# Kernel optimization log

Measured on AMD Instinct MI355X. Metric: run time of the kernel, lower is better.

The kernel has to match this reference:

```python
import jax, jax.numpy as jnp
import numpy as np

B, R, C_M, C_Z, H, DH, NQP = 2, 384, 384, 128, 12, 32, 4
W_C = (2.0 / (9 * NQP)) ** (-0.5)   # (2/(9*n_qp))^-0.5
W_L = 3.0 ** 0.5                     # (1/3)^-0.5


def setup_inputs() -> dict:
    key = jax.random.key(0)
    ks = jax.random.split(key, 10)
    pair_rep = jax.random.normal(ks[0], (B, R, R, C_Z), jnp.float32)
    sing_rep = jax.random.normal(ks[1], (B, R, C_M), jnp.float32)
    m = jax.random.normal(ks[2], (B, R, 3, 3), jnp.float32)
    bbr, _ = jnp.linalg.qr(m)  # orthonormal backbone frames (B,R,3,3)
    bbt = jax.random.normal(ks[3], (B, R, 3), jnp.float32)
    s = 0.02
    W_qkv = jax.random.normal(ks[4], (C_M, DH * 3 * H), jnp.float32) * s
    W_qk = jax.random.normal(ks[5], (C_M, H * 2 * NQP * 3), jnp.float32) * s
    W_fc1 = jax.random.normal(ks[6], (C_Z, H), jnp.float32) * s
    b_fc1 = jnp.zeros((H,), jnp.float32)
    W0 = jax.random.normal(ks[7], (H * DH, C_M), jnp.float32) * s
    W1 = jax.random.normal(ks[8], (H * C_Z, C_M), jnp.float32) * s
    gamma = jax.random.uniform(ks[9], (1,), jnp.float32)
    return dict(pair_rep=pair_rep, sing_rep=sing_rep, bbr=bbr, bbt=bbt,
                W_qkv=W_qkv, W_qk=W_qk, W_fc1=W_fc1, b_fc1=b_fc1,
                W0=W0, W1=W1, gamma=gamma)


def reference(pair_rep, sing_rep, bbr, bbt, W_qkv, W_qk, W_fc1, b_fc1, W0, W1, gamma):
    # pair bias: fc1 then b i j h -> b h i j
    pair_bias = jnp.transpose(jnp.einsum('bijc,ch->bijh', pair_rep, W_fc1) + b_fc1,
                              (0, 3, 1, 2))                      # b h i j
    # scalar q/k/v: channel layout (dim_head, 3, heads)
    qkv = (sing_rep @ W_qkv).reshape(B, R, DH, 3, H)
    rq, rk, rv = (jnp.transpose(qkv[:, :, :, i, :], (0, 3, 1, 2)) for i in range(3))  # b h r d
    dot = jnp.einsum('bhid,bhjd->bhij', rq, rk) * DH ** (-0.5)
    # point q/k: channel layout (heads, 2, n_qp, 3)
    qk = (sing_rep @ W_qk).reshape(B, R, H, 2, NQP, 3)
    gq = jnp.transpose(qk[:, :, :, 0], (0, 3, 1, 2, 4))          # b p r h a
    gk = jnp.transpose(qk[:, :, :, 1], (0, 3, 1, 2, 4))
    # frame-transformed query/key points
    Tq = jnp.einsum('bprha,brak->phbrk', gq, bbr) + bbt          # p h b r 3
    Tk = jnp.einsum('bprha,brak->phbrk', gk, bbr) + bbt
    diff = Tq[:, :, :, :, None, :] - Tk[:, :, :, None, :, :]     # p h b i j 3
    sq = jnp.transpose(jnp.sum(diff * diff, axis=(0, -1)), (1, 0, 2, 3))  # b h i j
    head_w = jax.nn.softplus(gamma[0]) * W_C / 2                 # same scalar per head
    attn = jax.nn.softmax(W_L * (pair_bias + dot + head_w * sq), axis=-1)
    # pair-rep value aggregation -> W_1
    top = jnp.einsum('bhij,bijc->bihc', attn, pair_rep).reshape(B, R, H * C_Z) @ W1
    # scalar value aggregation -> W_0   (note: original adds these two only;
    # the point-value 'bot' branch is computed but unused in the output)
    out = jnp.transpose(jnp.einsum('bhij,bhjd->bhid', attn, rv),
                        (0, 2, 1, 3)).reshape(B, R, H * DH) @ W0
    return out + top
```

## Files before the change

kernel.cpp:

```cpp
#include <hip/hip_runtime.h>
#include <math.h>

#define Bb   2
#define Rr   384
#define CMd  384
#define CZ   128
#define Hh   12
#define DHd  32

#define WL           1.7320508075688772f
#define WC           4.242640687119285f
#define INV_SQRT_DH  0.17677669529663687f

#define SZ_R   (Bb*Hh*Rr*DHd)
#define SZ_T   (Bb*Hh*Rr*12)
#define SZ_S   (Bb*Hh*Rr)
#define SZ_A   ((long)Bb*Hh*Rr*Rr)
#define SZ_O   (Bb*Rr*Hh*DHd)
#define SZ_TOP (Bb*Rr*Hh*CZ)

__global__ __launch_bounds__(64) void k_projgemm(
    const float* __restrict__ sing, const float* __restrict__ Wqkv,
    const float* __restrict__ Wqk, float* __restrict__ pbuf)
{
  const int t = threadIdx.x;
  const int m0 = blockIdx.x * 32;
  const int n0 = blockIdx.y * 32;
  const int ks = blockIdx.z;
  const int tx = t & 7, ty = t >> 3;
  __shared__ float As[32][36];
  __shared__ float Bs[32][36];
  float acc[4][4] = {};

  for (int kc = ks*192; kc < ks*192 + 192; kc += 32) {
    #pragma unroll
    for (int i = 0; i < 4; ++i) {
      int s = t + 64*i;
      int row = s >> 3, k4 = (s & 7) << 2;
      float4 v = *(const float4*)(sing + (long)(m0 + row)*384 + kc + k4);
      As[k4  ][row] = v.x; As[k4+1][row] = v.y;
      As[k4+2][row] = v.z; As[k4+3][row] = v.w;
    }
    #pragma unroll
    for (int i = 0; i < 4; ++i) {
      int s = t + 64*i;
      int k = s >> 3, c4 = (s & 7) << 2;
      const float* srcB = (n0 < 1152)
          ? Wqkv + (long)(kc + k)*1152 + n0 + c4
          : Wqk  + (long)(kc + k)*288 + (n0 - 1152) + c4;
      float4 w = *(const float4*)srcB;
      Bs[k][c4] = w.x; Bs[k][c4+1] = w.y; Bs[k][c4+2] = w.z; Bs[k][c4+3] = w.w;
    }
    __syncthreads();
    #pragma unroll
    for (int k = 0; k < 32; ++k) {
      float4 a = *(const float4*)&As[k][ty*4];
      float4 b = *(const float4*)&Bs[k][tx*4];
      acc[0][0] += a.x*b.x; acc[0][1] += a.x*b.y; acc[0][2] += a.x*b.z; acc[0][3] += a.x*b.w;
      acc[1][0] += a.y*b.x; acc[1][1] += a.y*b.y; acc[1][2] += a.y*b.z; acc[1][3] += a.y*b.w;
      acc[2][0] += a.z*b.x; acc[2][1] += a.z*b.y; acc[2][2] += a.z*b.z; acc[2][3] += a.z*b.w;
      acc[3][0] += a.w*b.x; acc[3][1] += a.w*b.y; acc[3][2] += a.w*b.z; acc[3][3] += a.w*b.w;
    }
    __syncthreads();
  }
  float* pd = pbuf + (long)ks * (768*1440);
  #pragma unroll
  for (int i = 0; i < 4; ++i)
    *(float4*)&pd[(long)(m0 + ty*4 + i)*1440 + n0 + tx*4] =
        make_float4(acc[i][0], acc[i][1], acc[i][2], acc[i][3]);
}

__global__ __launch_bounds__(256) void k_scatter(
    const float* __restrict__ pbuf,
    float* __restrict__ rq, float* __restrict__ rk, float* __restrict__ rv,
    float* __restrict__ rvT, float* __restrict__ gbuf)
{
  const int idx = blockIdx.x*256 + threadIdx.x;
  const int row = idx / 360;
  const int n   = (idx - row*360) * 4;
  float4 a = ((const float4*)pbuf)[idx];
  float4 b = ((const float4*)(pbuf + (long)768*1440))[idx];
  float v[4] = {a.x + b.x, a.y + b.y, a.z + b.z, a.w + b.w};
  const int bb = row / Rr, rr = row - bb*Rr;
  #pragma unroll
  for (int j = 0; j < 4; ++j) {
    int nj = n + j;
    if (nj < 1152) {
      int d = nj/36, rem = nj - d*36, wh = rem/12, h = rem - wh*12;
      float* dst = (wh == 0) ? rq : (wh == 1) ? rk : rv;
      dst[(((long)bb*Hh + h)*Rr + rr)*DHd + d] = v[j];
      if (wh == 2)
        rvT[(((long)bb*Hh + h)*DHd + d)*Rr + rr] = v[j];
    } else {
      gbuf[(long)row*288 + nj - 1152] = v[j];
    }
  }
}

__global__ __launch_bounds__(256) void k_frame(
    const float* __restrict__ gbuf, const float* __restrict__ bbr,
    const float* __restrict__ bbt,
    float* __restrict__ TqF, float* __restrict__ TkF,
    float* __restrict__ Qsq, float* __restrict__ Ksq)
{
  const int idx = blockIdx.x*256 + threadIdx.x;
  const int row = idx / 24, q = idx - row*24;
  const int h = q >> 1, s2 = q & 1;
  const float* gp = gbuf + (long)row*288 + h*24 + s2*12;
  float rot[9], tr[3];
  #pragma unroll
  for (int a = 0; a < 9; ++a) rot[a] = bbr[(long)row*9 + a];
  #pragma unroll
  for (int a = 0; a < 3; ++a) tr[a] = bbt[(long)row*3 + a];
  const int b = row / Rr, r = row - b*Rr;
  float* T = s2 ? TkF : TqF;
  const long tb = (((long)b*Hh + h)*Rr + r)*12;
  float v[12]; float ss = 0.f;
  #pragma unroll
  for (int p = 0; p < 4; ++p)
    #pragma unroll
    for (int k2 = 0; k2 < 3; ++k2) {
      float x = gp[p*3+0]*rot[k2] + gp[p*3+1]*rot[3+k2] + gp[p*3+2]*rot[6+k2] + tr[k2];
      v[p*3+k2] = x; ss += x*x;
    }
  *(float4*)(T + tb)     = make_float4(v[0], v[1], v[2],  v[3]);
  *(float4*)(T + tb + 4) = make_float4(v[4], v[5], v[6],  v[7]);
  *(float4*)(T + tb + 8) = make_float4(v[8], v[9], v[10], v[11]);
  (s2 ? Ksq : Qsq)[((long)b*Hh + h)*Rr + r] = ss;
}

__global__ __launch_bounds__(256) void k_pbias(
    const float* __restrict__ pair, const float* __restrict__ Wfc1,
    const float* __restrict__ bfc1, float* __restrict__ pb)
{
  const int t = threadIdx.x;
  const long base = (long)blockIdx.x * 64;
  __shared__ float tile[64][129];
  __shared__ float w_l[128][12];
  __shared__ float bias_l[12];
  for (int idx = t; idx < 128*12; idx += 256) w_l[idx/12][idx%12] = Wfc1[idx];
  if (t < 12) bias_l[t] = bfc1[t];
  const float4* src = (const float4*)(pair + base*CZ);
  for (int idx = t; idx < 64*32; idx += 256) {
    float4 v = src[idx];
    int row = idx >> 5, c4 = (idx & 31) << 2;
    tile[row][c4] = v.x; tile[row][c4+1] = v.y; tile[row][c4+2] = v.z; tile[row][c4+3] = v.w;
  }
  __syncthreads();
  int row = t & 63;
  long n = base + row;
  int b = (int)(n / ((long)Rr*Rr));
  long rr2 = n - (long)b*Rr*Rr;
  int i = (int)(rr2 / Rr), j = (int)(rr2 - (long)i*Rr);
  int h0 = t >> 6;
  float a0 = bias_l[h0], a1 = bias_l[h0+4], a2 = bias_l[h0+8];
  for (int c = 0; c < 128; ++c) {
    float v = tile[row][c];
    a0 += v*w_l[c][h0]; a1 += v*w_l[c][h0+4]; a2 += v*w_l[c][h0+8];
  }
  long o = (((long)b*Hh + h0)*Rr + i)*Rr + j;
  const long hstride = (long)Rr*Rr*4;
  pb[o] = a0; pb[o + hstride] = a1; pb[o + 2*hstride] = a2;
}

#define ITILE 8
__global__ __launch_bounds__(256) void k_scores(
    const float* __restrict__ rq, const float* __restrict__ rk,
    const float* __restrict__ TqF, const float* __restrict__ TkF,
    const float* __restrict__ Qsq, const float* __restrict__ Ksq,
    const float* __restrict__ gamma, float* __restrict__ attn)
{
  const int t = threadIdx.x;
  const int nt = Rr / ITILE;
  const int bh = blockIdx.x / nt;
  const int i0 = (blockIdx.x - bh*nt) * ITILE;
  __shared__ __align__(16) float rkf[384*32];
  __shared__ __align__(16) float rq_l[32];
  __shared__ float tq_l[12];
  __shared__ float scal[1];
  __shared__ float redm[4], reds[4];

  for (int idx = t; idx < 384*32; idx += 256) {
    int j = idx >> 5, dd = idx & 31;
    int q = dd >> 2, e = dd & 3;
    rkf[(j << 5) + (((q ^ (j & 7)) << 2) | e)] = rk[(long)bh*Rr*DHd + idx];
  }

  const float g0 = gamma[0];
  const float head_w = log1pf(__expf(g0)) * (WC * 0.5f);

  for (int ii = 0; ii < ITILE; ++ii) {
    const int i = i0 + ii;
    if (t < 32) rq_l[t] = rq[((long)bh*Rr + i)*DHd + t];
    if (t < 12) tq_l[t] = TqF[((long)bh*Rr + i)*12 + t];
    if (t == 0) scal[0] = Qsq[(long)bh*Rr + i];
    __syncthreads();
    const float qs = scal[0];
    const long rowbase = ((long)bh*Rr + i)*Rr;

    auto logit_at = [&](int j) -> float {
      const float* rkrow = &rkf[j << 5];
      const int sw = j & 7;
      float dt = 0.f;
      #pragma unroll
      for (int q = 0; q < 8; ++q) {
        float4 kv = *(const float4*)&rkrow[(q ^ sw) << 2];
        float4 qv = *(const float4*)&rq_l[q << 2];
        dt += kv.x*qv.x + kv.y*qv.y + kv.z*qv.z + kv.w*qv.w;
      }
      const float4* tk = (const float4*)(TkF + ((long)bh*Rr + j)*12);
      float4 ta = tk[0], tb = tk[1], tc = tk[2];
      float pt = tq_l[0]*ta.x + tq_l[1]*ta.y + tq_l[2]*ta.z + tq_l[3]*ta.w
               + tq_l[4]*tb.x + tq_l[5]*tb.y + tq_l[6]*tb.z + tq_l[7]*tb.w
               + tq_l[8]*tc.x + tq_l[9]*tc.y + tq_l[10]*tc.z + tq_l[11]*tc.w;
      float sqv = qs + Ksq[(long)bh*Rr + j] - 2.f*pt;
      return WL * (attn[rowbase + j] + dt*INV_SQRT_DH + head_w*sqv);
    };

    float l0 = logit_at(t);
    float l1 = (t < 128) ? logit_at(t + 256) : -3.4e38f;
    float m = fmaxf(l0, l1);
    #pragma unroll
    for (int s = 32; s; s >>= 1) m = fmaxf(m, __shfl_xor(m, s, 64));
    if ((t & 63) == 0) redm[t >> 6] = m;
    __syncthreads();
    m = fmaxf(fmaxf(redm[0], redm[1]), fmaxf(redm[2], redm[3]));
    float e0 = __expf(l0 - m);
    float e1 = (t < 128) ? __expf(l1 - m) : 0.f;
    float s = e0 + e1;
    #pragma unroll
    for (int sh = 32; sh; sh >>= 1) s += __shfl_xor(s, sh, 64);
    if ((t & 63) == 0) reds[t >> 6] = s;
    __syncthreads();
    float inv = 1.f / (reds[0] + reds[1] + reds[2] + reds[3]);
    attn[rowbase + t] = e0 * inv;
    if (t < 128) attn[rowbase + t + 256] = e1 * inv;
    __syncthreads();
  }
}

__global__ __launch_bounds__(256) void k_agg(
    const float* __restrict__ attn, const float* __restrict__ pair,
    const float* __restrict__ rvT, float* __restrict__ o_ihd, float* __restrict__ top)
{
  const int t = threadIdx.x;
  const int bi = blockIdx.x;
  const int b = bi / Rr;
  const int i = bi - b*Rr;
  __shared__ __align__(16) float a_l[12][384];
  for (int idx = t; idx < 12*384; idx += 256) {
    int h = idx / 384, j = idx - h*384;
    a_l[h][j] = attn[(((long)b*Hh + h)*Rr + i)*Rr + j];
  }
  __syncthreads();
  const int c = t & 127, hh = t >> 7;
  const float* prow = pair + (long)bi * Rr * CZ;
  float acc0=0,acc1=0,acc2=0,acc3=0,acc4=0,acc5=0;
  #pragma unroll 8
  for (int j = 0; j < 384; ++j) {
    float v = prow[(long)j*CZ + c];
    acc0 += a_l[hh   ][j]*v;
    acc1 += a_l[hh+2 ][j]*v;
    acc2 += a_l[hh+4 ][j]*v;
    acc3 += a_l[hh+6 ][j]*v;
    acc4 += a_l[hh+8 ][j]*v;
    acc5 += a_l[hh+10][j]*v;
  }
  float* tp = top + ((long)bi*Hh)*CZ + c;
  tp[(long)(hh   )*CZ] = acc0;
  tp[(long)(hh+2 )*CZ] = acc1;
  tp[(long)(hh+4 )*CZ] = acc2;
  tp[(long)(hh+6 )*CZ] = acc3;
  tp[(long)(hh+8 )*CZ] = acc4;
  tp[(long)(hh+10)*CZ] = acc5;
  for (int o = t; o < 384; o += 256) {
    int h = o >> 5, dd = o & 31;
    const float* rp = rvT + (((long)b*Hh + h)*DHd + dd)*Rr;
    float s = 0.f;
    #pragma unroll 4
    for (int j4 = 0; j4 < 96; ++j4) {
      float4 rv4 = *(const float4*)&rp[j4*4];
      float4 av  = *(const float4*)&a_l[h][j4*4];
      s += rv4.x*av.x + rv4.y*av.y + rv4.z*av.z + rv4.w*av.w;
    }
    o_ihd[(long)bi*384 + o] = s;
  }
}

#define K5_KSPLIT 6
#define K5_KLEN   320
__global__ __launch_bounds__(64) void k_final_part(
    const float* __restrict__ o_ihd, const float* __restrict__ top,
    const float* __restrict__ W0, const float* __restrict__ W1,
    float* __restrict__ partial)
{
  const int t = threadIdx.x;
  const int m0 = blockIdx.x * 32;
  const int n0 = blockIdx.y * 32;
  const int ks = blockIdx.z;
  const int tx = t & 7, ty = t >> 3;
  __shared__ float As[32][36];
  __shared__ float Bs[32][36];
  float acc[4][4] = {};

  for (int kc = ks*K5_KLEN; kc < ks*K5_KLEN + K5_KLEN; kc += 32) {
    #pragma unroll
    for (int i = 0; i < 4; ++i) {
      int s = t + 64*i;
      int row = s >> 3, k4 = (s & 7) << 2;
      int gk = kc + k4;
      const float* srcA = (gk < 384)
          ? o_ihd + (long)(m0 + row)*384 + gk
          : top   + (long)(m0 + row)*1536 + (gk - 384);
      float4 v = *(const float4*)srcA;
      As[k4  ][row] = v.x; As[k4+1][row] = v.y;
      As[k4+2][row] = v.z; As[k4+3][row] = v.w;
    }
    #pragma unroll
    for (int i = 0; i < 4; ++i) {
      int s = t + 64*i;
      int k = s >> 3, c4 = (s & 7) << 2;
      int gk = kc + k;
      const float* srcB = (gk < 384)
          ? W0 + (long)gk*384 + n0 + c4
          : W1 + (long)(gk - 384)*384 + n0 + c4;
      float4 w = *(const float4*)srcB;
      Bs[k][c4] = w.x; Bs[k][c4+1] = w.y; Bs[k][c4+2] = w.z; Bs[k][c4+3] = w.w;
    }
    __syncthreads();
    #pragma unroll
    for (int k = 0; k < 32; ++k) {
      float4 a = *(const float4*)&As[k][ty*4];
      float4 b = *(const float4*)&Bs[k][tx*4];
      acc[0][0] += a.x*b.x; acc[0][1] += a.x*b.y; acc[0][2] += a.x*b.z; acc[0][3] += a.x*b.w;
      acc[1][0] += a.y*b.x; acc[1][1] += a.y*b.y; acc[1][2] += a.y*b.z; acc[1][3] += a.y*b.w;
      acc[2][0] += a.z*b.x; acc[2][1] += a.z*b.y; acc[2][2] += a.z*b.z; acc[2][3] += a.z*b.w;
      acc[3][0] += a.w*b.x; acc[3][1] += a.w*b.y; acc[3][2] += a.w*b.z; acc[3][3] += a.w*b.w;
    }
    __syncthreads();
  }
  float* pdst = partial + (long)ks * (768*384);
  #pragma unroll
  for (int i = 0; i < 4; ++i)
    *(float4*)&pdst[(long)(m0 + ty*4 + i)*384 + n0 + tx*4] =
        make_float4(acc[i][0], acc[i][1], acc[i][2], acc[i][3]);
}

__global__ __launch_bounds__(256) void k_final_reduce(
    const float* __restrict__ partial, float* __restrict__ out)
{
  const int idx = blockIdx.x*256 + threadIdx.x;
  float4 r = make_float4(0.f, 0.f, 0.f, 0.f);
  #pragma unroll
  for (int p = 0; p < K5_KSPLIT; ++p) {
    float4 a = ((const float4*)(partial + (long)p*768*384))[idx];
    r.x += a.x; r.y += a.y; r.z += a.z; r.w += a.w;
  }
  ((float4*)out)[idx] = r;
}

extern "C" void kernel_launch(void* const* d_in, const int* in_sizes, int n_in,
                              void* d_out, int out_size, void* d_ws, size_t ws_size,
                              hipStream_t stream)
{
  (void)in_sizes; (void)n_in; (void)out_size; (void)ws_size;
  const float* pair  = (const float*)d_in[0];
  const float* sing  = (const float*)d_in[1];
  const float* bbr   = (const float*)d_in[2];
  const float* bbt   = (const float*)d_in[3];
  const float* Wqkv  = (const float*)d_in[4];
  const float* Wqk   = (const float*)d_in[5];
  const float* Wfc1  = (const float*)d_in[6];
  const float* bfc1  = (const float*)d_in[7];
  const float* W0    = (const float*)d_in[8];
  const float* W1    = (const float*)d_in[9];
  const float* gamma = (const float*)d_in[10];
  float* out = (float*)d_out;

  float* ws    = (float*)d_ws;
  float* rq    = ws;
  float* rk    = rq  + SZ_R;
  float* rv    = rk  + SZ_R;
  float* TqF   = rv  + SZ_R;
  float* TkF   = TqF + SZ_T;
  float* Qsq   = TkF + SZ_T;
  float* Ksq   = Qsq + SZ_S;
  float* attn  = Ksq + SZ_S;
  float* o_ihd = attn + SZ_A;
  float* top   = o_ihd + SZ_O;
  float* rvT   = top + SZ_TOP;
  float* gbuf  = o_ihd;
  float* pbuf  = attn;
  float* partial = attn;

  k_projgemm<<<dim3(24, 45, 2), dim3(64), 0, stream>>>(sing, Wqkv, Wqk, pbuf);
  k_scatter<<<dim3(276480/256), dim3(256), 0, stream>>>(pbuf, rq, rk, rv, rvT, gbuf);
  k_frame<<<dim3(Bb*Rr*24/256), dim3(256), 0, stream>>>(
      gbuf, bbr, bbt, TqF, TkF, Qsq, Ksq);
  k_pbias<<<dim3(Bb*Rr*Rr/64), dim3(256), 0, stream>>>(pair, Wfc1, bfc1, attn);
  k_scores<<<dim3(Bb*Hh*(Rr/ITILE)), dim3(256), 0, stream>>>(
      rq, rk, TqF, TkF, Qsq, Ksq, gamma, attn);
  k_agg<<<dim3(Bb*Rr), dim3(256), 0, stream>>>(attn, pair, rvT, o_ihd, top);
  k_final_part<<<dim3(24, 12, K5_KSPLIT), dim3(64), 0, stream>>>(
      o_ihd, top, W0, W1, partial);
  k_final_reduce<<<dim3(768*384/4/256), dim3(256), 0, stream>>>(partial, out);
}
```

Measured before the change: 231.5 us.

## Restructure pair aggregation with float4 loads, j-split threads, and tree reduction

The pair-value aggregation kernel now gives each thread a float4 of channels and one eighth of the j range, keeping 12 head accumulators per thread. Partial sums are combined across the 8 j-groups through a shared-memory tree reduction before the float4 store. This is meant to widen global loads and cut redundant reads of the pair row, at the cost of 48 accumulator registers, extra shared memory and several barriers. Separately, the scores kernel swaps the XOR-swizzled float4 rk layout for a padded [384][33] scalar layout.

```diff
diff --git a/kernel.cpp b/kernel.cpp
--- a/kernel.cpp
+++ b/kernel.cpp
@@ -174,17 +174,14 @@
   const int nt = Rr / ITILE;
   const int bh = blockIdx.x / nt;
   const int i0 = (blockIdx.x - bh*nt) * ITILE;
-  __shared__ __align__(16) float rkf[384*32];
-  __shared__ __align__(16) float rq_l[32];
+  __shared__ float rk_l[384][33];
+  __shared__ float rq_l[32];
   __shared__ float tq_l[12];
   __shared__ float scal[1];
   __shared__ float redm[4], reds[4];
 
-  for (int idx = t; idx < 384*32; idx += 256) {
-    int j = idx >> 5, dd = idx & 31;
-    int q = dd >> 2, e = dd & 3;
-    rkf[(j << 5) + (((q ^ (j & 7)) << 2) | e)] = rk[(long)bh*Rr*DHd + idx];
-  }
+  for (int idx = t; idx < 384*32; idx += 256)
+    rk_l[idx >> 5][idx & 31] = rk[(long)bh*Rr*DHd + idx];
 
   const float g0 = gamma[0];
   const float head_w = log1pf(__expf(g0)) * (WC * 0.5f);
@@ -199,15 +196,9 @@
     const long rowbase = ((long)bh*Rr + i)*Rr;
 
     auto logit_at = [&](int j) -> float {
-      const float* rkrow = &rkf[j << 5];
-      const int sw = j & 7;
       float dt = 0.f;
       #pragma unroll
-      for (int q = 0; q < 8; ++q) {
-        float4 kv = *(const float4*)&rkrow[(q ^ sw) << 2];
-        float4 qv = *(const float4*)&rq_l[q << 2];
-        dt += kv.x*qv.x + kv.y*qv.y + kv.z*qv.z + kv.w*qv.w;
-      }
+      for (int dd = 0; dd < 32; ++dd) dt += rq_l[dd] * rk_l[j][dd];
       const float4* tk = (const float4*)(TkF + ((long)bh*Rr + j)*12);
       float4 ta = tk[0], tb = tk[1], tc = tk[2];
       float pt = tq_l[0]*ta.x + tq_l[1]*ta.y + tq_l[2]*ta.z + tq_l[3]*ta.w
@@ -248,31 +239,68 @@
   const int b = bi / Rr;
   const int i = bi - b*Rr;
   __shared__ __align__(16) float a_l[12][384];
+  __shared__ __align__(16) float4 red[4][12][32];
   for (int idx = t; idx < 12*384; idx += 256) {
     int h = idx / 384, j = idx - h*384;
     a_l[h][j] = attn[(((long)b*Hh + h)*Rr + i)*Rr + j];
   }
   __syncthreads();
-  const int c = t & 127, hh = t >> 7;
-  const float* prow = pair + (long)bi * Rr * CZ;
-  float acc0=0,acc1=0,acc2=0,acc3=0,acc4=0,acc5=0;
-  #pragma unroll 8
-  for (int j = 0; j < 384; ++j) {
-    float v = prow[(long)j*CZ + c];
-    acc0 += a_l[hh   ][j]*v;
-    acc1 += a_l[hh+2 ][j]*v;
-    acc2 += a_l[hh+4 ][j]*v;
-    acc3 += a_l[hh+6 ][j]*v;
-    acc4 += a_l[hh+8 ][j]*v;
-    acc5 += a_l[hh+10][j]*v;
-  }
-  float* tp = top + ((long)bi*Hh)*CZ + c;
-  tp[(long)(hh   )*CZ] = acc0;
-  tp[(long)(hh+2 )*CZ] = acc1;
-  tp[(long)(hh+4 )*CZ] = acc2;
-  tp[(long)(hh+6 )*CZ] = acc3;
-  tp[(long)(hh+8 )*CZ] = acc4;
-  tp[(long)(hh+10)*CZ] = acc5;
+  const int c4 = t & 31;
+  const int jg = t >> 5;
+  const float4* prow4 = (const float4*)(pair + (long)bi * Rr * CZ);
+  float4 acc[12];
+  #pragma unroll
+  for (int h = 0; h < 12; ++h) acc[h] = make_float4(0.f, 0.f, 0.f, 0.f);
+  #pragma unroll 4
+  for (int k = 0; k < 48; ++k) {
+    const int j = jg + (k << 3);
+    float4 pv = prow4[j*32 + c4];
+    #pragma unroll
+    for (int h = 0; h < 12; ++h) {
+      float a = a_l[h][j];
+      acc[h].x += a*pv.x; acc[h].y += a*pv.y; acc[h].z += a*pv.z; acc[h].w += a*pv.w;
+    }
+  }
+  __syncthreads();
+  if (jg >= 4) {
+    #pragma unroll
+    for (int h = 0; h < 12; ++h) red[jg-4][h][c4] = acc[h];
+  }
+  __syncthreads();
+  if (jg < 4) {
+    #pragma unroll
+    for (int h = 0; h < 12; ++h) {
+      float4 r = red[jg][h][c4];
+      acc[h].x += r.x; acc[h].y += r.y; acc[h].z += r.z; acc[h].w += r.w;
+    }
+  }
+  __syncthreads();
+  if (jg == 2 || jg == 3) {
+    #pragma unroll
+    for (int h = 0; h < 12; ++h) red[jg-2][h][c4] = acc[h];
+  }
+  __syncthreads();
+  if (jg < 2) {
+    #pragma unroll
+    for (int h = 0; h < 12; ++h) {
+      float4 r = red[jg][h][c4];
+      acc[h].x += r.x; acc[h].y += r.y; acc[h].z += r.z; acc[h].w += r.w;
+    }
+  }
+  __syncthreads();
+  if (jg == 1) {
+    #pragma unroll
+    for (int h = 0; h < 12; ++h) red[0][h][c4] = acc[h];
+  }
+  __syncthreads();
+  if (jg == 0) {
+    #pragma unroll
+    for (int h = 0; h < 12; ++h) {
+      float4 r = red[0][h][c4];
+      acc[h].x += r.x; acc[h].y += r.y; acc[h].z += r.z; acc[h].w += r.w;
+      *(float4*)&top[((long)bi*Hh + h)*CZ + c4*4] = acc[h];
+    }
+  }
   for (int o = t; o < 384; o += 256) {
     int h = o >> 5, dd = o & 31;
     const float* rp = rvT + (((long)b*Hh + h)*DHd + dd)*Rr;
```

Result: no change. 233.7 us (+1.0%).
